# Optimization experiments

Hardware: AMD Instinct MI355X
Metric: run time of the kernel (lower is better)

The kernel has to match this reference:

```python
import jax, jax.numpy as jnp
import numpy as np

B, D, K = 8192, 1024, 30


def _sample_neg_indices(key, batch_size, num_negs):
    # per-row uniform indices in [0, 2B) excluding {i, i+B}, matching _sample_negatives
    total = 2 * batch_size
    i = jnp.arange(batch_size)[:, None]                      # [B,1]
    r = jax.random.randint(key, (batch_size, num_negs), 0, total - 2)
    a = r + (r >= i)                                         # skip index i
    b = a + (a >= (i + batch_size))                          # skip index i+B
    return b.astype(jnp.int32)


def setup_inputs() -> dict:
    key = jax.random.key(0)
    k1, k2, k3 = jax.random.split(key, 3)
    return {
        "z_i": jax.random.normal(k1, (B, D), dtype=jnp.float32),
        "z_j": jax.random.normal(k2, (B, D), dtype=jnp.float32),
        "temperature": jnp.asarray(0.2, dtype=jnp.float32),
        "neg_indices": _sample_neg_indices(k3, B, K),        # [B,K] int32
    }


def _l2_normalize(x, eps=1e-12):
    # matches F.normalize(p=2, dim=1): x / max(||x||, eps)
    n = jnp.sqrt(jnp.sum(x * x, axis=1, keepdims=True))
    return x / jnp.maximum(n, eps)


def reference(z_i, z_j, temperature, neg_indices):
    zi = _l2_normalize(z_i)                                  # [B,D]
    zj = _l2_normalize(z_j)                                  # [B,D]
    pos_sim = jnp.sum(zi * zj, axis=1)                       # [B]
    pool = jnp.concatenate([zi, zj], axis=0)                 # [2B,D]
    z_neg = pool[neg_indices]                                # [B,K,D] irregular gather
    neg_sim = jnp.einsum("bd,bkd->bk", zi, z_neg)            # [B,K]
    logits = jnp.concatenate([pos_sim[:, None], neg_sim], axis=1) / temperature  # [B,1+K]
    # cross entropy with labels == 0
    loss = -jnp.mean(jax.nn.log_softmax(logits, axis=1)[:, 0])
    return loss
```

## Files before the change

kernel.cpp:

```cpp
#include <hip/hip_runtime.h>
#include <math.h>

constexpr int NB = 8192;
constexpr int ND = 1024;
constexpr int NK = 30;
constexpr int RS = ND / 4;

#if defined(__has_builtin)
#  if __has_builtin(__builtin_amdgcn_sdot4)
#    define HAVE_SDOT4 1
#  endif
#endif
#ifndef HAVE_SDOT4
#  define HAVE_SDOT4 0
#endif

__device__ __forceinline__ int SDOT4(int a, int b, int acc) {
#if HAVE_SDOT4
    return __builtin_amdgcn_sdot4(a, b, acc, false);
#else
    return acc + (int)(signed char)(a)        * (int)(signed char)(b)
               + (int)(signed char)(a >> 8)   * (int)(signed char)(b >> 8)
               + (int)(signed char)(a >> 16)  * (int)(signed char)(b >> 16)
               + (int)(a >> 24)               * (int)(b >> 24);
#endif
}

__device__ __forceinline__ int pack4_i8(float a, float b, float c, float d) {
    int x0 = (int)rintf(a), x1 = (int)rintf(b), x2 = (int)rintf(c), x3 = (int)rintf(d);
    return (x0 & 255) | ((x1 & 255) << 8) | ((x2 & 255) << 16) | (x3 << 24);
}

__global__ void normalize_i8_kernel(const float* __restrict__ zi,
                                    const float* __restrict__ zj,
                                    int* __restrict__ pool) {
    int row  = blockIdx.x * 4 + (threadIdx.x >> 6);
    int lane = threadIdx.x & 63;
    const float* src = (row < NB) ? (zi + (size_t)row * ND)
                                  : (zj + (size_t)(row - NB) * ND);
    float v[16];
    float s = 0.f;
#pragma unroll
    for (int seg = 0; seg < 4; ++seg) {
        float4 t = *reinterpret_cast<const float4*>(src + lane * 16 + seg * 4);
        v[seg * 4 + 0] = t.x; v[seg * 4 + 1] = t.y;
        v[seg * 4 + 2] = t.z; v[seg * 4 + 3] = t.w;
        s += t.x * t.x + t.y * t.y + t.z * t.z + t.w * t.w;
    }
#pragma unroll
    for (int off = 32; off >= 1; off >>= 1)
        s += __shfl_xor(s, off, 64);
    float inv = 127.f / fmaxf(sqrtf(s), 1e-12f);

    int4 w;
    w.x = pack4_i8(v[0]*inv,  v[1]*inv,  v[2]*inv,  v[3]*inv);
    w.y = pack4_i8(v[4]*inv,  v[5]*inv,  v[6]*inv,  v[7]*inv);
    w.z = pack4_i8(v[8]*inv,  v[9]*inv,  v[10]*inv, v[11]*inv);
    w.w = pack4_i8(v[12]*inv, v[13]*inv, v[14]*inv, v[15]*inv);
    *reinterpret_cast<int4*>(pool + (size_t)row * RS + lane * 4) = w;
}

__global__ void loss_chunk_kernel(const int* __restrict__ pool,
                                  const int* __restrict__ neg_idx,
                                  int* __restrict__ partial) {
    int wave = threadIdx.x >> 6;
    int lane = threadIdx.x & 63;
    int c    = blockIdx.x & 7;
    int row  = (blockIdx.x >> 3) * 4 + wave;
    int g    = lane >> 3;
    int p    = lane & 7;

    const int* cbase = pool + c * 32 + p * 4;

    int4 a4 = *reinterpret_cast<const int4*>(cbase + (size_t)row * RS);

    int myidx = (lane < NK) ? neg_idx[row * NK + lane] : 0;

    int4 b4[4];
#pragma unroll
    for (int t = 0; t < 4; ++t) {
        int s = t * 8 + g;
        int r = (s == 0) ? (row + NB)
              : (s < 31) ? __shfl(myidx, s - 1, 64)
                         : 0;
        b4[t] = *reinterpret_cast<const int4*>(cbase + (size_t)r * RS);
    }

    int d0 = 0, d1 = 0, d2 = 0, d3 = 0;
    d0 = SDOT4(a4.x, b4[0].x, d0); d0 = SDOT4(a4.y, b4[0].y, d0);
    d0 = SDOT4(a4.z, b4[0].z, d0); d0 = SDOT4(a4.w, b4[0].w, d0);
    d1 = SDOT4(a4.x, b4[1].x, d1); d1 = SDOT4(a4.y, b4[1].y, d1);
    d1 = SDOT4(a4.z, b4[1].z, d1); d1 = SDOT4(a4.w, b4[1].w, d1);
    d2 = SDOT4(a4.x, b4[2].x, d2); d2 = SDOT4(a4.y, b4[2].y, d2);
    d2 = SDOT4(a4.z, b4[2].z, d2); d2 = SDOT4(a4.w, b4[2].w, d2);
    d3 = SDOT4(a4.x, b4[3].x, d3); d3 = SDOT4(a4.y, b4[3].y, d3);
    d3 = SDOT4(a4.z, b4[3].z, d3); d3 = SDOT4(a4.w, b4[3].w, d3);

#pragma unroll
    for (int off = 1; off <= 4; off <<= 1) {
        d0 += __shfl_xor(d0, off, 64);
        d1 += __shfl_xor(d1, off, 64);
        d2 += __shfl_xor(d2, off, 64);
        d3 += __shfl_xor(d3, off, 64);
    }

    if (p < 4) {
        int val = (p == 0) ? d0 : (p == 1) ? d1 : (p == 2) ? d2 : d3;
        partial[(size_t)row * 256 + c * 32 + p * 8 + g] = val;
    }
}

__global__ void lse_kernel(const int* __restrict__ partial,
                           const float* __restrict__ temp_ptr,
                           float* __restrict__ block_part) {
    int wave = threadIdx.x >> 6;
    int lane = threadIdx.x & 63;
    int row  = blockIdx.x * 4 + wave;

    float inv_t = 1.f / (127.f * 127.f * temp_ptr[0]);

    int4 v = *reinterpret_cast<const int4*>(partial + (size_t)row * 256 + lane * 4);
    int s0 = v.x, s1 = v.y, s2 = v.z, s3 = v.w;
#pragma unroll
    for (int off = 8; off <= 32; off <<= 1) {
        s0 += __shfl_xor(s0, off, 64);
        s1 += __shfl_xor(s1, off, 64);
        s2 += __shfl_xor(s2, off, 64);
        s3 += __shfl_xor(s3, off, 64);
    }
    float l0 = s0 * inv_t, l1 = s1 * inv_t, l2 = s2 * inv_t, l3 = s3 * inv_t;
    if ((lane & 7) == 7) l3 = -1e30f;

    float m = fmaxf(fmaxf(l0, l1), fmaxf(l2, l3));
#pragma unroll
    for (int off = 1; off <= 4; off <<= 1)
        m = fmaxf(m, __shfl_xor(m, off, 64));

    float e = __expf(l0 - m) + __expf(l1 - m) + __expf(l2 - m) + __expf(l3 - m);
#pragma unroll
    for (int off = 1; off <= 4; off <<= 1)
        e += __shfl_xor(e, off, 64);

    float logit0 = __shfl(l0, lane & 56, 64);
    float loss = (m + logf(e)) - logit0;

    __shared__ float red[4];
    if (lane == 0) red[wave] = loss;
    __syncthreads();
    if (threadIdx.x == 0)
        block_part[blockIdx.x] = red[0] + red[1] + red[2] + red[3];
}

__global__ void reduce_kernel(const float* __restrict__ partial, int n,
                              float* __restrict__ out) {
    float s = 0.f;
    for (int i = threadIdx.x; i < n; i += 256) s += partial[i];
#pragma unroll
    for (int off = 32; off >= 1; off >>= 1)
        s += __shfl_xor(s, off, 64);
    __shared__ float lds[4];
    int wave = threadIdx.x >> 6, lane = threadIdx.x & 63;
    if (lane == 0) lds[wave] = s;
    __syncthreads();
    if (threadIdx.x == 0)
        out[0] = (lds[0] + lds[1] + lds[2] + lds[3]) * (1.f / (float)NB);
}

__global__ void norms_kernel(const float* __restrict__ zi,
                             const float* __restrict__ zj,
                             float* __restrict__ inv_norm) {
    int row  = blockIdx.x * 4 + (threadIdx.x >> 6);
    int lane = threadIdx.x & 63;
    if (row >= 2 * NB) return;
    const float* src = (row < NB) ? (zi + (size_t)row * ND)
                                  : (zj + (size_t)(row - NB) * ND);
    float s = 0.f;
#pragma unroll
    for (int seg = 0; seg < 4; ++seg) {
        float4 v = *reinterpret_cast<const float4*>(src + seg * 256 + lane * 4);
        s += v.x*v.x + v.y*v.y + v.z*v.z + v.w*v.w;
    }
#pragma unroll
    for (int off = 32; off >= 1; off >>= 1)
        s += __shfl_xor(s, off, 64);
    if (lane == 0)
        inv_norm[row] = 1.f / fmaxf(sqrtf(s), 1e-12f);
}

__global__ void loss_kernel_f32(const float* __restrict__ zi,
                                const float* __restrict__ zj,
                                const int*   __restrict__ neg_idx,
                                const float* __restrict__ temp_ptr,
                                const float* __restrict__ inv_norm,
                                float* __restrict__ partial) {
    int wave = threadIdx.x >> 6;
    int lane = threadIdx.x & 63;
    int row  = blockIdx.x * 4 + wave;
    float inv_t = 1.f / temp_ptr[0];
    const float* a = zi + (size_t)row * ND;
    float4 av[4];
#pragma unroll
    for (int seg = 0; seg < 4; ++seg)
        av[seg] = *reinterpret_cast<const float4*>(a + seg * 256 + lane * 4);
    float inv_a = inv_norm[row];
    float m = -INFINITY, ssum = 0.f, logit0 = 0.f;
    for (int k = -1; k < NK; ++k) {
        int r = (k < 0) ? (row + NB) : neg_idx[row * NK + k];
        const float* bp = (r < NB) ? (zi + (size_t)r * ND)
                                   : (zj + (size_t)(r - NB) * ND);
        float inv_b = inv_norm[r];
        float dot = 0.f;
#pragma unroll
        for (int seg = 0; seg < 4; ++seg) {
            float4 bv = *reinterpret_cast<const float4*>(bp + seg * 256 + lane * 4);
            dot += av[seg].x*bv.x + av[seg].y*bv.y + av[seg].z*bv.z + av[seg].w*bv.w;
        }
#pragma unroll
        for (int off = 32; off >= 1; off >>= 1)
            dot += __shfl_xor(dot, off, 64);
        float logit = dot * inv_a * inv_b * inv_t;
        if (k < 0) logit0 = logit;
        if (logit > m) { ssum = ssum * __expf(m - logit) + 1.f; m = logit; }
        else           { ssum += __expf(logit - m); }
    }
    float loss = (m + logf(ssum)) - logit0;
    __shared__ float red[4];
    if (lane == 0) red[wave] = loss;
    __syncthreads();
    if (threadIdx.x == 0)
        partial[blockIdx.x] = red[0] + red[1] + red[2] + red[3];
}

extern "C" void kernel_launch(void* const* d_in, const int* in_sizes, int n_in,
                              void* d_out, int out_size, void* d_ws, size_t ws_size,
                              hipStream_t stream) {
    const float* zi      = (const float*)d_in[0];
    const float* zj      = (const float*)d_in[1];
    const float* temp    = (const float*)d_in[2];
    const int*   neg_idx = (const int*)d_in[3];
    float* out = (float*)d_out;

    const size_t pool_bytes  = (size_t)2 * NB * ND;
    const size_t part_bytes  = (size_t)NB * 256 * sizeof(int);
    const size_t block_bytes = (size_t)(NB / 4) * sizeof(float);

    if (ws_size >= pool_bytes + part_bytes + block_bytes) {
        int*   pool       = (int*)d_ws;
        int*   partial    = (int*)((char*)d_ws + pool_bytes);
        float* block_part = (float*)((char*)d_ws + pool_bytes + part_bytes);

        normalize_i8_kernel<<<(2 * NB) / 4, 256, 0, stream>>>(zi, zj, pool);
        loss_chunk_kernel<<<(NB / 4) * 8, 256, 0, stream>>>(pool, neg_idx, partial);
        lse_kernel<<<NB / 4, 256, 0, stream>>>(partial, temp, block_part);
        reduce_kernel<<<1, 256, 0, stream>>>(block_part, NB / 4, out);
    } else {
        float* inv_norm = (float*)d_ws;
        float* partial  = inv_norm + 2 * NB;

        norms_kernel<<<(2 * NB) / 4, 256, 0, stream>>>(zi, zj, inv_norm);
        loss_kernel_f32<<<NB / 4, 256, 0, stream>>>(zi, zj, neg_idx, temp,
                                                    inv_norm, partial);
        reduce_kernel<<<1, 256, 0, stream>>>(partial, NB / 4, out);
    }
}
```

Measured before the change: 41.69 us.

## Accumulate chunk dot products with atomics into compact per-row logits

Each of the 8 D-chunks now atomically adds its partial dot product into a 32-slot-per-row int logits buffer, replacing the 256-int-per-row partial buffer. The normalize kernel zeroes that buffer, and the LSE kernel processes two rows per wave with a 32-lane reduction, using half as many blocks. This shrinks intermediate writes and reads roughly eightfold, at the cost of int atomic contention on the same addresses across chunk blocks. Integer atomics keep the result deterministic.

```diff
diff --git a/kernel.cpp b/kernel.cpp
--- a/kernel.cpp
+++ b/kernel.cpp
@@ -33,7 +33,11 @@
 
 __global__ void normalize_i8_kernel(const float* __restrict__ zi,
                                     const float* __restrict__ zj,
-                                    int* __restrict__ pool) {
+                                    int* __restrict__ pool,
+                                    int* __restrict__ logits) {
+    if (threadIdx.x < 64)
+        logits[blockIdx.x * 64 + threadIdx.x] = 0;
+
     int row  = blockIdx.x * 4 + (threadIdx.x >> 6);
     int lane = threadIdx.x & 63;
     const float* src = (row < NB) ? (zi + (size_t)row * ND)
@@ -62,7 +66,7 @@
 
 __global__ void loss_chunk_kernel(const int* __restrict__ pool,
                                   const int* __restrict__ neg_idx,
-                                  int* __restrict__ partial) {
+                                  int* __restrict__ logits) {
     int wave = threadIdx.x >> 6;
     int lane = threadIdx.x & 63;
     int c    = blockIdx.x & 7;
@@ -70,11 +74,10 @@
     int g    = lane >> 3;
     int p    = lane & 7;
 
+    int myidx = (lane < NK) ? neg_idx[row * NK + lane] : 0;
+
     const int* cbase = pool + c * 32 + p * 4;
-
     int4 a4 = *reinterpret_cast<const int4*>(cbase + (size_t)row * RS);
-
-    int myidx = (lane < NK) ? neg_idx[row * NK + lane] : 0;
 
     int4 b4[4];
 #pragma unroll
@@ -106,46 +109,37 @@
 
     if (p < 4) {
         int val = (p == 0) ? d0 : (p == 1) ? d1 : (p == 2) ? d2 : d3;
-        partial[(size_t)row * 256 + c * 32 + p * 8 + g] = val;
-    }
-}
-
-__global__ void lse_kernel(const int* __restrict__ partial,
+        atomicAdd(&logits[row * 32 + p * 8 + g], val);
+    }
+}
+
+__global__ void lse_kernel(const int* __restrict__ logits,
                            const float* __restrict__ temp_ptr,
                            float* __restrict__ block_part) {
     int wave = threadIdx.x >> 6;
     int lane = threadIdx.x & 63;
-    int row  = blockIdx.x * 4 + wave;
+    int slot = lane & 31;
+    int row  = blockIdx.x * 8 + wave * 2 + (lane >> 5);
 
     float inv_t = 1.f / (127.f * 127.f * temp_ptr[0]);
 
-    int4 v = *reinterpret_cast<const int4*>(partial + (size_t)row * 256 + lane * 4);
-    int s0 = v.x, s1 = v.y, s2 = v.z, s3 = v.w;
-#pragma unroll
-    for (int off = 8; off <= 32; off <<= 1) {
-        s0 += __shfl_xor(s0, off, 64);
-        s1 += __shfl_xor(s1, off, 64);
-        s2 += __shfl_xor(s2, off, 64);
-        s3 += __shfl_xor(s3, off, 64);
-    }
-    float l0 = s0 * inv_t, l1 = s1 * inv_t, l2 = s2 * inv_t, l3 = s3 * inv_t;
-    if ((lane & 7) == 7) l3 = -1e30f;
-
-    float m = fmaxf(fmaxf(l0, l1), fmaxf(l2, l3));
-#pragma unroll
-    for (int off = 1; off <= 4; off <<= 1)
+    float l = (slot < 31) ? logits[row * 32 + slot] * inv_t : -1e30f;
+
+    float m = l;
+#pragma unroll
+    for (int off = 1; off <= 16; off <<= 1)
         m = fmaxf(m, __shfl_xor(m, off, 64));
-
-    float e = __expf(l0 - m) + __expf(l1 - m) + __expf(l2 - m) + __expf(l3 - m);
-#pragma unroll
-    for (int off = 1; off <= 4; off <<= 1)
+    float e = __expf(l - m);
+#pragma unroll
+    for (int off = 1; off <= 16; off <<= 1)
         e += __shfl_xor(e, off, 64);
 
-    float logit0 = __shfl(l0, lane & 56, 64);
-    float loss = (m + logf(e)) - logit0;
+    float l0   = __shfl(l, lane & 32, 64);
+    float loss = (m + logf(e)) - l0;
+    float loss2 = __shfl(loss, 32, 64);
 
     __shared__ float red[4];
-    if (lane == 0) red[wave] = loss;
+    if (lane == 0) red[wave] = loss + loss2;
     __syncthreads();
     if (threadIdx.x == 0)
         block_part[blockIdx.x] = red[0] + red[1] + red[2] + red[3];
@@ -240,19 +234,19 @@
     const int*   neg_idx = (const int*)d_in[3];
     float* out = (float*)d_out;
 
-    const size_t pool_bytes  = (size_t)2 * NB * ND;
-    const size_t part_bytes  = (size_t)NB * 256 * sizeof(int);
-    const size_t block_bytes = (size_t)(NB / 4) * sizeof(float);
-
-    if (ws_size >= pool_bytes + part_bytes + block_bytes) {
+    const size_t pool_bytes   = (size_t)2 * NB * ND;
+    const size_t logits_bytes = (size_t)NB * 32 * sizeof(int);
+    const size_t block_bytes  = (size_t)(NB / 8) * sizeof(float);
+
+    if (ws_size >= pool_bytes + logits_bytes + block_bytes) {
         int*   pool       = (int*)d_ws;
-        int*   partial    = (int*)((char*)d_ws + pool_bytes);
-        float* block_part = (float*)((char*)d_ws + pool_bytes + part_bytes);
-
-        normalize_i8_kernel<<<(2 * NB) / 4, 256, 0, stream>>>(zi, zj, pool);
-        loss_chunk_kernel<<<(NB / 4) * 8, 256, 0, stream>>>(pool, neg_idx, partial);
-        lse_kernel<<<NB / 4, 256, 0, stream>>>(partial, temp, block_part);
-        reduce_kernel<<<1, 256, 0, stream>>>(block_part, NB / 4, out);
+        int*   logits     = (int*)((char*)d_ws + pool_bytes);
+        float* block_part = (float*)((char*)d_ws + pool_bytes + logits_bytes);
+
+        normalize_i8_kernel<<<(2 * NB) / 4, 256, 0, stream>>>(zi, zj, pool, logits);
+        loss_chunk_kernel<<<(NB / 4) * 8, 256, 0, stream>>>(pool, neg_idx, logits);
+        lse_kernel<<<NB / 8, 256, 0, stream>>>(logits, temp, block_part);
+        reduce_kernel<<<1, 256, 0, stream>>>(block_part, NB / 8, out);
     } else {
         float* inv_norm = (float*)d_ws;
         float* partial  = inv_norm + 2 * NB;
```

After: 40.34 us. 1.03x faster.
